# Kernel tuning notes

Hardware: AMD Instinct MI355X
Metric: run time of the kernel (lower is better)

## Reference

```python
import jax, jax.numpy as jnp
import numpy as np

WIN = 9  # window_size (isotropic, module default)
EPS = 1e-5


def _box_sum3d(x, win):
    """Sum over a win^3 box, same-size output ('same' padding). x: [B,1,D,H,W].
    The ones kernel is separable, so apply three 1D convolutions."""
    pad = win // 2
    for ax in range(3):  # spatial axes D,H,W
        kshape = [1, 1, 1, 1, 1]
        kshape[2 + ax] = win
        k = jnp.ones(kshape, x.dtype)
        padding = [(0, 0)] * 3
        padding[ax] = (pad, pad)
        x = jax.lax.conv_general_dilated(x, k, window_strides=(1, 1, 1), padding=padding)
    return x


def setup_inputs() -> dict:
    key = jax.random.key(0)
    k1, k2 = jax.random.split(key)
    shape = (2, 1, 160, 192, 160)
    y_pred = jax.random.normal(k1, shape, dtype=jnp.float32)
    y_true = jax.random.normal(k2, shape, dtype=jnp.float32)
    return {"y_pred": y_pred, "y_true": y_true}


def reference(y_pred, y_true):
    I, J = y_true, y_pred
    win_size = jnp.asarray(WIN ** 3, I.dtype)  # 729

    I_sum = _box_sum3d(I, WIN)
    J_sum = _box_sum3d(J, WIN)
    I2_sum = _box_sum3d(I * I, WIN)
    J2_sum = _box_sum3d(J * J, WIN)
    IJ_sum = _box_sum3d(I * J, WIN)

    I_mean = I_sum / win_size
    J_mean = J_sum / win_size

    cross = IJ_sum - J_mean * I_sum - I_mean * J_sum + I_mean * J_mean * win_size
    I_var = I2_sum - 2 * I_mean * I_sum + I_mean * I_mean * win_size
    J_var = J2_sum - 2 * J_mean * J_sum + J_mean * J_mean * win_size

    cc = cross * cross / (I_var * J_var + EPS)
    return -jnp.mean(cc)
```

## Files before the change

### kernel.cpp

```cpp
#include <hip/hip_runtime.h>


#define B_    2
#define D_    160
#define H_    192
#define W_    160
#define HW_   (H_*W_)
#define SSTR  28
#define SSLC  (24*SSTR)
#define OFF_J (2*SSLC)
#define OFF_WS 2688
#define WFS   484
#define WSLC5 (5*WFS)
#define OFF_HS (OFF_WS + 2*WSLC5)
#define HFS   324
#define HSLC5 (5*HFS)
#define OFF_RED (OFF_HS + 2*HSLC5)
#define SMEM_TOT (OFF_RED + 8)
#define DC    40
#define NMAC  24
#define W3I   (1.0f/729.0f)
#define NTOT  9830400.0f

#if __has_builtin(__builtin_amdgcn_rcpf)
#define RCP(x) __builtin_amdgcn_rcpf(x)
#else
#define RCP(x) (1.0f/(x))
#endif

#define LGKM0() asm volatile("s_waitcnt lgkmcnt(0)" ::: "memory")

#define SLIDEX(EXPR, F) { \
  float v_[12]; \
  _Pragma("unroll") for (int k_ = 0; k_ < 12; ++k_) { v_[k_] = (EXPR); } \
  float s_ = v_[0]+v_[1]+v_[2]+v_[3]+v_[4]+v_[5]+v_[6]+v_[7]+v_[8]; \
  float4 o_; o_.x = s_; s_ += v_[9]-v_[0]; o_.y = s_; \
  s_ += v_[10]-v_[1]; o_.z = s_; s_ += v_[11]-v_[2]; o_.w = s_; \
  *(float4*)&sm[wwr + (F)*WFS] = o_; }

__global__ __launch_bounds__(256, 3) void ncc_fused(const float* __restrict__ gI,
                                                    const float* __restrict__ gJ,
                                                    float* __restrict__ out)
{
  __shared__ __align__(16) float sm[SMEM_TOT];
  const int tid  = threadIdx.x;
  const int lane = tid & 63;
  const int Q    = tid >> 6;
  const int w0   = blockIdx.x * 16;
  const int h0   = blockIdx.y * 16;
  const int bz   = blockIdx.z;
  const int bb   = bz >> 2;
  const int d_lo = (bz & 3) * DC;

  for (int i = tid; i < OFF_WS; i += 256) sm[i] = 0.f;

  bool val0 = false, val1 = false;
  int  lds0 = 0, lds1 = 0, slc0 = 0, slc1 = 0;
  const float *pi0 = gI, *pj0 = gJ, *pi1 = gI, *pj1 = gJ;
  {
    const int tA = tid;
    const int tB = (tid >= 224) ? (tid + 32) : 512;
    auto prep = [&](int t, bool& val, int& lo, int& slc,
                    const float*& pi, const float*& pj) {
      if (t >= 288) { val = false; return; }
      slc = t / 144;
      const int u = t - slc*144;
      const int r = u / 6, c = u - r*6;
      const int gh = h0 - 4 + r;
      const int gw = w0 - 4 + 4*c;
      val = ((unsigned)gh < (unsigned)H_) && (gw >= 0) && (gw + 3 < W_);
      lo  = slc*SSLC + r*SSTR + 4*c;
      const long off = ((long)(bb*D_ + (d_lo - 4 + slc))*H_ + gh)*(long)W_ + gw;
      pi = gI + off; pj = gJ + off;
    };
    prep(tA, val0, lds0, slc0, pi0, pj0);
    prep(tB, val1, lds1, slc1, pi1, pj1);
  }

  const bool wact = (lane < 48);
  const int  wslc = lane / 24;
  const int  wrow = lane - wslc*24;
  const int  wrd  = wslc*SSLC + wrow*SSTR + 4*Q;
  const int  wwr  = OFF_WS + wslc*WSLC5 + wrow*20 + 4*Q;

  auto prep_h = [&](int t, int& rd, int& wr) {
    const int wq   = t & 3;
    const int f    = (t >> 2) % 5;
    const int half = (t / 20) & 1;
    const int slc  = t / 40;
    rd = OFF_WS + slc*WSLC5 + f*WFS + half*160 + 4*Q + wq;
    wr = OFF_HS + slc*HSLC5 + f*HFS + half*160 + 4*Q + wq;
  };
  int h1rd, h1wr, h2rd = 0, h2wr = 0;
  prep_h(lane, h1rd, h1wr);
  const bool hact2 = (lane < 16);
  if (hact2) prep_h(lane + 64, h2rd, h2wr);

  const int rh = lane >> 2, rwq = lane & 3;
  const int hbA = OFF_HS + rh*20 + 4*Q + rwq;
  const int hbB = hbA + HSLC5;

  float ring[5][9], S[5];
  #pragma unroll
  for (int f = 0; f < 5; ++f) {
    S[f] = 0.f;
    #pragma unroll
    for (int k = 0; k < 9; ++k) ring[f][k] = 0.f;
  }
  float acc = 0.f;

  float4 f0i = {0,0,0,0}, f0j = {0,0,0,0}, f1i = {0,0,0,0}, f1j = {0,0,0,0};
  auto fetch = [&](int sbase) {
    if (val0 && (unsigned)(sbase + slc0) < (unsigned)D_) {
      f0i = *(const float4*)pi0; f0j = *(const float4*)pj0;
    } else { f0i = make_float4(0,0,0,0); f0j = make_float4(0,0,0,0); }
    pi0 += 2*HW_; pj0 += 2*HW_;
    if (val1 && (unsigned)(sbase + slc1) < (unsigned)D_) {
      f1i = *(const float4*)pi1; f1j = *(const float4*)pj1;
    } else { f1i = make_float4(0,0,0,0); f1j = make_float4(0,0,0,0); }
    pi1 += 2*HW_; pj1 += 2*HW_;
  };
  auto stage_write = [&]() {
    if (val0) { *(float4*)&sm[lds0] = f0i; *(float4*)&sm[lds0 + OFF_J] = f0j; }
    if (val1) { *(float4*)&sm[lds1] = f1i; *(float4*)&sm[lds1 + OFF_J] = f1j; }
  };

  auto ring_cc = [&](int mu) {
    float nA[5], nB[5];
    #pragma unroll
    for (int f = 0; f < 5; ++f) { nA[f] = sm[hbA + f*HFS]; nB[f] = sm[hbB + f*HFS]; }
    float SA[5], SB[5];
    #pragma unroll
    for (int f = 0; f < 5; ++f) {
      SA[f] = S[f]  + nA[f] - ring[f][8];
      SB[f] = SA[f] + nB[f] - ring[f][7];
      S[f]  = SB[f];
      #pragma unroll
      for (int k = 8; k >= 2; --k) ring[f][k] = ring[f][k-2];
      ring[f][1] = nA[f]; ring[f][0] = nB[f];
    }
    if (mu >= 4) {
      {
        const float cr = SA[4] - SA[0]*SA[1]*W3I;
        const float vi = SA[2] - SA[0]*SA[0]*W3I;
        const float vj = SA[3] - SA[1]*SA[1]*W3I;
        acc += cr*cr * RCP(vi*vj + 1e-5f);
      }
      {
        const float cr = SB[4] - SB[0]*SB[1]*W3I;
        const float vi = SB[2] - SB[0]*SB[0]*W3I;
        const float vj = SB[3] - SB[1]*SB[1]*W3I;
        acc += cr*cr * RCP(vi*vj + 1e-5f);
      }
    }
  };

  fetch(d_lo - 4);
  __syncthreads();
  stage_write();
  __syncthreads();

  int sA = d_lo - 4;
  for (int m = 0; m < NMAC; ++m, sA += 2) {
    if (m + 1 < NMAC) fetch(sA + 2);

    if (m > 0) ring_cc(m - 1);

    if (wact) {
      const float4 a0 = *(const float4*)&sm[wrd];
      const float4 a1 = *(const float4*)&sm[wrd + 4];
      const float4 a2 = *(const float4*)&sm[wrd + 8];
      const float4 b0 = *(const float4*)&sm[wrd + OFF_J];
      const float4 b1 = *(const float4*)&sm[wrd + OFF_J + 4];
      const float4 b2 = *(const float4*)&sm[wrd + OFF_J + 8];
      const float wi[12] = {a0.x,a0.y,a0.z,a0.w,a1.x,a1.y,a1.z,a1.w,a2.x,a2.y,a2.z,a2.w};
      const float wj[12] = {b0.x,b0.y,b0.z,b0.w,b1.x,b1.y,b1.z,b1.w,b2.x,b2.y,b2.z,b2.w};
      SLIDEX(wi[k_],        0)
      SLIDEX(wj[k_],        1)
      SLIDEX(wi[k_]*wi[k_], 2)
      SLIDEX(wj[k_]*wj[k_], 3)
      SLIDEX(wi[k_]*wj[k_], 4)
    }
    LGKM0();

    {
      auto hrun = [&](int rd, int wr) {
        float v[16];
        #pragma unroll
        for (int k = 0; k < 16; ++k) v[k] = sm[rd + k*20];
        float s = v[0]+v[1]+v[2]+v[3]+v[4]+v[5]+v[6]+v[7]+v[8];
        sm[wr] = s;
        #pragma unroll
        for (int j = 1; j < 8; ++j) { s += v[j+8] - v[j-1]; sm[wr + j*20] = s; }
      };
      hrun(h1rd, h1wr);
      if (hact2) hrun(h2rd, h2wr);
    }

    __syncthreads();
    if (m + 1 < NMAC) stage_write();
    __syncthreads();
  }

  ring_cc(NMAC - 1);

  float v = acc;
  #pragma unroll
  for (int off = 32; off > 0; off >>= 1)
    v += __shfl_down(v, off, 64);
  if (lane == 0) sm[OFF_RED + Q] = v;
  __syncthreads();
  if (tid == 0) {
    const float t = sm[OFF_RED] + sm[OFF_RED+1] + sm[OFF_RED+2] + sm[OFF_RED+3];
    atomicAdd(out, -t / NTOT);
  }
}

extern "C" void kernel_launch(void* const* d_in, const int* in_sizes, int n_in,
                              void* d_out, int out_size, void* d_ws, size_t ws_size,
                              hipStream_t stream) {
  const float* J = (const float*)d_in[0];
  const float* I = (const float*)d_in[1];
  float* outp = (float*)d_out;
  hipMemsetAsync(d_out, 0, sizeof(float), stream);
  dim3 grid(W_/16, H_/16, B_*4);
  ncc_fused<<<grid, dim3(256), 0, stream>>>(I, J, outp);
}
```

Before: 174.6 us.

## Store W/H partial box sums as fp16 in LDS and use packed half2 H-pass

Converts the W-direction partial sums to packed fp16 before writing them to shared memory. The H-direction sliding sum now runs with packed half2 add/sub on fewer lanes, and the D-ring reads back single halves. The D-ring/cc step moves into the same iteration right after the H pass, and launch bounds rise to 4 blocks/SM because LDS use shrinks. This cuts LDS footprint and traffic and halves H-pass ALU work. The cost is large precision loss: the I², J² and IJ sums and the variance subtractions lose accuracy in fp16, which may break the tolerance.

Result: faster. 151.3 us (-13.3%).

```diff
diff --git a/kernel.cpp b/kernel.cpp
--- a/kernel.cpp
+++ b/kernel.cpp
@@ -1,4 +1,5 @@
 #include <hip/hip_runtime.h>
+#include <hip/hip_fp16.h>
 
 
 #define B_    2
@@ -10,12 +11,14 @@
 #define SSLC  (24*SSTR)
 #define OFF_J (2*SSLC)
 #define OFF_WS 2688
-#define WFS   484
-#define WSLC5 (5*WFS)
-#define OFF_HS (OFF_WS + 2*WSLC5)
-#define HFS   324
-#define HSLC5 (5*HFS)
-#define OFF_RED (OFF_HS + 2*HSLC5)
+#define WROW  10
+#define WSLC2 240
+#define WFS2  486
+#define OFF_HS (OFF_WS + 5*WFS2)
+#define HROW  10
+#define HSLC2 160
+#define HFS2  326
+#define OFF_RED (OFF_HS + 5*HFS2)
 #define SMEM_TOT (OFF_RED + 8)
 #define DC    40
 #define NMAC  24
@@ -29,6 +32,8 @@
 #endif
 
 #define LGKM0() asm volatile("s_waitcnt lgkmcnt(0)" ::: "memory")
+
+struct __align__(8) Half2x2 { __half2 a, b; };
 
 #define SLIDEX(EXPR, F) { \
   float v_[12]; \
@@ -36,9 +41,11 @@
   float s_ = v_[0]+v_[1]+v_[2]+v_[3]+v_[4]+v_[5]+v_[6]+v_[7]+v_[8]; \
   float4 o_; o_.x = s_; s_ += v_[9]-v_[0]; o_.y = s_; \
   s_ += v_[10]-v_[1]; o_.z = s_; s_ += v_[11]-v_[2]; o_.w = s_; \
-  *(float4*)&sm[wwr + (F)*WFS] = o_; }
-
-__global__ __launch_bounds__(256, 3) void ncc_fused(const float* __restrict__ gI,
+  Half2x2 pk_; pk_.a = __floats2half2_rn(o_.x, o_.y); \
+  pk_.b = __floats2half2_rn(o_.z, o_.w); \
+  *(Half2x2*)&sm[wwr + (F)*WFS2] = pk_; }
+
+__global__ __launch_bounds__(256, 4) void ncc_fused(const float* __restrict__ gI,
                                                     const float* __restrict__ gJ,
                                                     float* __restrict__ out)
 {
@@ -78,27 +85,26 @@
   }
 
   const bool wact = (lane < 48);
-  const int  wslc = lane / 24;
-  const int  wrow = lane - wslc*24;
+  const int  wslc = (lane >= 24) ? 1 : 0;
+  const int  wrow = lane - 24*wslc;
   const int  wrd  = wslc*SSLC + wrow*SSTR + 4*Q;
-  const int  wwr  = OFF_WS + wslc*WSLC5 + wrow*20 + 4*Q;
-
-  auto prep_h = [&](int t, int& rd, int& wr) {
-    const int wq   = t & 3;
-    const int f    = (t >> 2) % 5;
-    const int half = (t / 20) & 1;
-    const int slc  = t / 40;
-    rd = OFF_WS + slc*WSLC5 + f*WFS + half*160 + 4*Q + wq;
-    wr = OFF_HS + slc*HSLC5 + f*HFS + half*160 + 4*Q + wq;
-  };
-  int h1rd, h1wr, h2rd = 0, h2wr = 0;
-  prep_h(lane, h1rd, h1wr);
-  const bool hact2 = (lane < 16);
-  if (hact2) prep_h(lane + 64, h2rd, h2wr);
+  const int  wwr  = OFF_WS + wslc*WSLC2 + wrow*WROW + 2*Q;
+
+  const bool hact = (lane < 40);
+  int hrd = 0, hwr = 0;
+  {
+    const int t     = hact ? lane : 0;
+    const int wpair = t & 1;
+    const int f     = (t >> 1) % 5;
+    const int half  = (t / 10) & 1;
+    const int slc   = t / 20;
+    hrd = OFF_WS + f*WFS2 + slc*WSLC2 + half*(8*WROW) + 2*Q + wpair;
+    hwr = OFF_HS + f*HFS2 + slc*HSLC2 + half*(8*HROW) + 2*Q + wpair;
+  }
 
   const int rh = lane >> 2, rwq = lane & 3;
-  const int hbA = OFF_HS + rh*20 + 4*Q + rwq;
-  const int hbB = hbA + HSLC5;
+  const int hb  = OFF_HS + rh*HROW + 2*Q + (rwq >> 1);
+  const int sh16 = (rwq & 1) * 16;
 
   float ring[5][9], S[5];
   #pragma unroll
@@ -125,34 +131,9 @@
     if (val1) { *(float4*)&sm[lds1] = f1i; *(float4*)&sm[lds1 + OFF_J] = f1j; }
   };
 
-  auto ring_cc = [&](int mu) {
-    float nA[5], nB[5];
-    #pragma unroll
-    for (int f = 0; f < 5; ++f) { nA[f] = sm[hbA + f*HFS]; nB[f] = sm[hbB + f*HFS]; }
-    float SA[5], SB[5];
-    #pragma unroll
-    for (int f = 0; f < 5; ++f) {
-      SA[f] = S[f]  + nA[f] - ring[f][8];
-      SB[f] = SA[f] + nB[f] - ring[f][7];
-      S[f]  = SB[f];
-      #pragma unroll
-      for (int k = 8; k >= 2; --k) ring[f][k] = ring[f][k-2];
-      ring[f][1] = nA[f]; ring[f][0] = nB[f];
-    }
-    if (mu >= 4) {
-      {
-        const float cr = SA[4] - SA[0]*SA[1]*W3I;
-        const float vi = SA[2] - SA[0]*SA[0]*W3I;
-        const float vj = SA[3] - SA[1]*SA[1]*W3I;
-        acc += cr*cr * RCP(vi*vj + 1e-5f);
-      }
-      {
-        const float cr = SB[4] - SB[0]*SB[1]*W3I;
-        const float vi = SB[2] - SB[0]*SB[0]*W3I;
-        const float vj = SB[3] - SB[1]*SB[1]*W3I;
-        acc += cr*cr * RCP(vi*vj + 1e-5f);
-      }
-    }
+  auto h2ext = [&](int addr) -> float {
+    const unsigned u = *(const unsigned*)&sm[addr];
+    return __half2float(__ushort_as_half((unsigned short)(u >> sh16)));
   };
 
   fetch(d_lo - 4);
@@ -163,8 +144,6 @@
   int sA = d_lo - 4;
   for (int m = 0; m < NMAC; ++m, sA += 2) {
     if (m + 1 < NMAC) fetch(sA + 2);
-
-    if (m > 0) ring_cc(m - 1);
 
     if (wact) {
       const float4 a0 = *(const float4*)&sm[wrd];
@@ -183,26 +162,60 @@
     }
     LGKM0();
 
+    if (hact) {
+      __half2 v[16];
+      #pragma unroll
+      for (int k = 0; k < 16; ++k) v[k] = *(const __half2*)&sm[hrd + k*WROW];
+      __half2 s = __hadd2(v[0], v[1]);
+      s = __hadd2(s, v[2]); s = __hadd2(s, v[3]); s = __hadd2(s, v[4]);
+      s = __hadd2(s, v[5]); s = __hadd2(s, v[6]); s = __hadd2(s, v[7]);
+      s = __hadd2(s, v[8]);
+      *(__half2*)&sm[hwr] = s;
+      #pragma unroll
+      for (int j = 1; j < 8; ++j) {
+        s = __hsub2(__hadd2(s, v[j+8]), v[j-1]);
+        *(__half2*)&sm[hwr + j*HROW] = s;
+      }
+    }
+    LGKM0();
+
     {
-      auto hrun = [&](int rd, int wr) {
-        float v[16];
+      float nA[5], nB[5];
+      #pragma unroll
+      for (int f = 0; f < 5; ++f) {
+        nA[f] = h2ext(hb + f*HFS2);
+        nB[f] = h2ext(hb + f*HFS2 + HSLC2);
+      }
+      float SA[5], SB[5];
+      #pragma unroll
+      for (int f = 0; f < 5; ++f) {
+        SA[f] = S[f]  + nA[f] - ring[f][8];
+        SB[f] = SA[f] + nB[f] - ring[f][7];
+        S[f]  = SB[f];
         #pragma unroll
-        for (int k = 0; k < 16; ++k) v[k] = sm[rd + k*20];
-        float s = v[0]+v[1]+v[2]+v[3]+v[4]+v[5]+v[6]+v[7]+v[8];
-        sm[wr] = s;
-        #pragma unroll
-        for (int j = 1; j < 8; ++j) { s += v[j+8] - v[j-1]; sm[wr + j*20] = s; }
-      };
-      hrun(h1rd, h1wr);
-      if (hact2) hrun(h2rd, h2wr);
+        for (int k = 8; k >= 2; --k) ring[f][k] = ring[f][k-2];
+        ring[f][1] = nA[f]; ring[f][0] = nB[f];
+      }
+      if (m >= 4) {
+        {
+          const float cr = SA[4] - SA[0]*SA[1]*W3I;
+          const float vi = SA[2] - SA[0]*SA[0]*W3I;
+          const float vj = SA[3] - SA[1]*SA[1]*W3I;
+          acc += cr*cr * RCP(vi*vj + 1e-5f);
+        }
+        {
+          const float cr = SB[4] - SB[0]*SB[1]*W3I;
+          const float vi = SB[2] - SB[0]*SB[0]*W3I;
+          const float vj = SB[3] - SB[1]*SB[1]*W3I;
+          acc += cr*cr * RCP(vi*vj + 1e-5f);
+        }
+      }
     }
 
     __syncthreads();
     if (m + 1 < NMAC) stage_write();
     __syncthreads();
   }
-
-  ring_cc(NMAC - 1);
 
   float v = acc;
   #pragma unroll
```

## Compute in-plane box sums with fp16 MFMA banded-matrix products

Applied to the files above, without the earlier changes.

Replaces the scalar sliding-window W and H box sums with 16x16x32 fp16 MFMA multiplications against a banded 0/1 selection matrix. Inputs and their products are converted to half precision when staged into shared memory, and intermediate sums are also kept in fp16. The goal is to move the dominant in-plane summation work onto matrix cores, shrink shared memory so occupancy can rise to 4 blocks, and double-buffer the global fetch across the loop. The cost is substantial precision loss: fp16 storage of squared values and of sums up to about 81 before variance subtraction risks catastrophic cancellation in the variance terms.

After: 147.5 us. 1.18x faster.

```diff
diff --git a/kernel.cpp b/kernel.cpp
--- a/kernel.cpp
+++ b/kernel.cpp
@@ -1,4 +1,5 @@
 #include <hip/hip_runtime.h>
+#include <hip/hip_fp16.h>
 
 
 #define B_    2
@@ -6,17 +7,18 @@
 #define H_    192
 #define W_    160
 #define HW_   (H_*W_)
-#define SSTR  28
-#define SSLC  (24*SSTR)
-#define OFF_J (2*SSLC)
-#define OFF_WS 2688
-#define WFS   484
-#define WSLC5 (5*WFS)
-#define OFF_HS (OFF_WS + 2*WSLC5)
-#define HFS   324
-#define HSLC5 (5*HFS)
-#define OFF_RED (OFF_HS + 2*HSLC5)
-#define SMEM_TOT (OFF_RED + 8)
+
+#define RS    20
+#define SLS   (24*RS)
+#define FS    (2*SLS)
+#define ZROW  4800
+#define TMP0  4816
+#define TS    20
+#define HSUM0 (TMP0 + 4*320)
+#define HCS   160
+#define HRS   10
+#define REDU  (HSUM0 + 10*HCS)
+#define SMEM  (REDU + 8)
 #define DC    40
 #define NMAC  24
 #define W3I   (1.0f/729.0f)
@@ -27,78 +29,74 @@
 #else
 #define RCP(x) (1.0f/(x))
 #endif
-
 #define LGKM0() asm volatile("s_waitcnt lgkmcnt(0)" ::: "memory")
 
-#define SLIDEX(EXPR, F) { \
-  float v_[12]; \
-  _Pragma("unroll") for (int k_ = 0; k_ < 12; ++k_) { v_[k_] = (EXPR); } \
-  float s_ = v_[0]+v_[1]+v_[2]+v_[3]+v_[4]+v_[5]+v_[6]+v_[7]+v_[8]; \
-  float4 o_; o_.x = s_; s_ += v_[9]-v_[0]; o_.y = s_; \
-  s_ += v_[10]-v_[1]; o_.z = s_; s_ += v_[11]-v_[2]; o_.w = s_; \
-  *(float4*)&sm[wwr + (F)*WFS] = o_; }
-
-__global__ __launch_bounds__(256, 3) void ncc_fused(const float* __restrict__ gI,
+typedef _Float16 half8 __attribute__((ext_vector_type(8)));
+typedef float    f32x4 __attribute__((ext_vector_type(4)));
+#define MFMA16(a,b,c) __builtin_amdgcn_mfma_f32_16x16x32_f16((a),(b),(c),0,0,0)
+
+struct __align__(8) HP { __half2 a, b; };
+
+__global__ __launch_bounds__(256, 4) void ncc_fused(const float* __restrict__ gI,
                                                     const float* __restrict__ gJ,
                                                     float* __restrict__ out)
 {
-  __shared__ __align__(16) float sm[SMEM_TOT];
+  __shared__ __align__(16) float sm[SMEM];
   const int tid  = threadIdx.x;
   const int lane = tid & 63;
   const int Q    = tid >> 6;
+  const int n15  = lane & 15;
+  const int q4   = lane >> 4;
   const int w0   = blockIdx.x * 16;
   const int h0   = blockIdx.y * 16;
   const int bz   = blockIdx.z;
   const int bb   = bz >> 2;
   const int d_lo = (bz & 3) * DC;
 
-  for (int i = tid; i < OFF_WS; i += 256) sm[i] = 0.f;
+  for (int i = tid; i < TMP0; i += 256) sm[i] = 0.f;
+
+  half8 SEL;
+  #pragma unroll
+  for (int j = 0; j < 8; ++j) {
+    const int k = 8*q4 + j;
+    SEL[j] = (k >= n15 && k <= n15 + 8) ? (_Float16)1 : (_Float16)0;
+  }
 
   bool val0 = false, val1 = false;
-  int  lds0 = 0, lds1 = 0, slc0 = 0, slc1 = 0;
+  int  lo0 = 0, lo1 = 0, sc0 = 0, sc1 = 0;
   const float *pi0 = gI, *pj0 = gJ, *pi1 = gI, *pj1 = gJ;
   {
-    const int tA = tid;
-    const int tB = (tid >= 224) ? (tid + 32) : 512;
-    auto prep = [&](int t, bool& val, int& lo, int& slc,
+    auto prep = [&](int t, bool& val, int& lo, int& sc,
                     const float*& pi, const float*& pj) {
       if (t >= 288) { val = false; return; }
-      slc = t / 144;
-      const int u = t - slc*144;
+      sc = t / 144;
+      const int u = t - sc*144;
       const int r = u / 6, c = u - r*6;
-      const int gh = h0 - 4 + r;
-      const int gw = w0 - 4 + 4*c;
+      const int gh = h0 - 4 + r, gw = w0 - 4 + 4*c;
       val = ((unsigned)gh < (unsigned)H_) && (gw >= 0) && (gw + 3 < W_);
-      lo  = slc*SSLC + r*SSTR + 4*c;
-      const long off = ((long)(bb*D_ + (d_lo - 4 + slc))*H_ + gh)*(long)W_ + gw;
+      lo  = sc*SLS + r*RS + 2*c;
+      const long off = ((long)(bb*D_ + (d_lo - 4 + sc))*H_ + gh)*(long)W_ + gw;
       pi = gI + off; pj = gJ + off;
     };
-    prep(tA, val0, lds0, slc0, pi0, pj0);
-    prep(tB, val1, lds1, slc1, pi1, pj1);
-  }
-
-  const bool wact = (lane < 48);
-  const int  wslc = lane / 24;
-  const int  wrow = lane - wslc*24;
-  const int  wrd  = wslc*SSLC + wrow*SSTR + 4*Q;
-  const int  wwr  = OFF_WS + wslc*WSLC5 + wrow*20 + 4*Q;
-
-  auto prep_h = [&](int t, int& rd, int& wr) {
-    const int wq   = t & 3;
-    const int f    = (t >> 2) % 5;
-    const int half = (t / 20) & 1;
-    const int slc  = t / 40;
-    rd = OFF_WS + slc*WSLC5 + f*WFS + half*160 + 4*Q + wq;
-    wr = OFF_HS + slc*HSLC5 + f*HFS + half*160 + 4*Q + wq;
-  };
-  int h1rd, h1wr, h2rd = 0, h2wr = 0;
-  prep_h(lane, h1rd, h1wr);
-  const bool hact2 = (lane < 16);
-  if (hact2) prep_h(lane + 64, h2rd, h2wr);
-
-  const int rh = lane >> 2, rwq = lane & 3;
-  const int hbA = OFF_HS + rh*20 + 4*Q + rwq;
-  const int hbB = hbA + HSLC5;
+    prep(tid, val0, lo0, sc0, pi0, pj0);
+    prep((tid >= 224) ? tid + 32 : 512, val1, lo1, sc1, pi1, pj1);
+  }
+
+  int rb_[3], hb_[3];
+  #pragma unroll
+  for (int i = 0; i < 3; ++i) {
+    int c = Q + 4*i; if (c > 9) c = 9;
+    rb_[i] = (c % 5)*FS + (c / 5)*SLS;
+    hb_[i] = HSUM0 + c*HCS;
+  }
+  const int tb  = TMP0 + Q*320 + n15*TS;
+  const int a1r = n15*RS + 4*q4;
+  const int a2r = (n15 < 8) ? ((16 + n15)*RS + 4*q4) : -1;
+  const int zr  = ZROW + 4*q4;
+
+  const int rh = tid >> 4, rw = tid & 15;
+  const int rbase = HSUM0 + rw*HRS + (rh >> 1);
+  const int rsh   = (rh & 1) * 16;
 
   float ring[5][9], S[5];
   #pragma unroll
@@ -111,24 +109,66 @@
 
   float4 f0i = {0,0,0,0}, f0j = {0,0,0,0}, f1i = {0,0,0,0}, f1j = {0,0,0,0};
   auto fetch = [&](int sbase) {
-    if (val0 && (unsigned)(sbase + slc0) < (unsigned)D_) {
+    if (val0 && (unsigned)(sbase + sc0) < (unsigned)D_) {
       f0i = *(const float4*)pi0; f0j = *(const float4*)pj0;
     } else { f0i = make_float4(0,0,0,0); f0j = make_float4(0,0,0,0); }
     pi0 += 2*HW_; pj0 += 2*HW_;
-    if (val1 && (unsigned)(sbase + slc1) < (unsigned)D_) {
+    if (val1 && (unsigned)(sbase + sc1) < (unsigned)D_) {
       f1i = *(const float4*)pi1; f1j = *(const float4*)pj1;
     } else { f1i = make_float4(0,0,0,0); f1j = make_float4(0,0,0,0); }
     pi1 += 2*HW_; pj1 += 2*HW_;
   };
+
+  auto stage_one = [&](int lo, float4 fi, float4 fj) {
+    const __half2 i01 = __floats2half2_rn(fi.x, fi.y);
+    const __half2 i23 = __floats2half2_rn(fi.z, fi.w);
+    const __half2 j01 = __floats2half2_rn(fj.x, fj.y);
+    const __half2 j23 = __floats2half2_rn(fj.z, fj.w);
+    HP hI; hI.a = i01; hI.b = i23;
+    HP hJ; hJ.a = j01; hJ.b = j23;
+    HP h2; h2.a = __hmul2(i01, i01); h2.b = __hmul2(i23, i23);
+    HP h3; h3.a = __hmul2(j01, j01); h3.b = __hmul2(j23, j23);
+    HP h4; h4.a = __hmul2(i01, j01); h4.b = __hmul2(i23, j23);
+    *(HP*)&sm[lo]        = hI;
+    *(HP*)&sm[lo +   FS] = hJ;
+    *(HP*)&sm[lo + 2*FS] = h2;
+    *(HP*)&sm[lo + 3*FS] = h3;
+    *(HP*)&sm[lo + 4*FS] = h4;
+  };
   auto stage_write = [&]() {
-    if (val0) { *(float4*)&sm[lds0] = f0i; *(float4*)&sm[lds0 + OFF_J] = f0j; }
-    if (val1) { *(float4*)&sm[lds1] = f1i; *(float4*)&sm[lds1 + OFF_J] = f1j; }
-  };
-
-  auto ring_cc = [&](int mu) {
+    if (val0) stage_one(lo0, f0i, f0j);
+    if (val1) stage_one(lo1, f1i, f1j);
+  };
+
+  auto chain = [&](int rb, int hb) {
+    const half8 A1 = *(const half8*)&sm[rb + a1r];
+    const half8 A2 = (a2r >= 0) ? *(const half8*)&sm[rb + a2r]
+                                : *(const half8*)&sm[zr];
+    const f32x4 z = {0.f, 0.f, 0.f, 0.f};
+    const f32x4 d1 = MFMA16(A1, SEL, z);
+    const f32x4 d2 = MFMA16(A2, SEL, z);
+    HP p1; p1.a = __floats2half2_rn(d1[0], d1[1]); p1.b = __floats2half2_rn(d1[2], d1[3]);
+    HP p2; p2.a = __floats2half2_rn(d2[0], d2[1]); p2.b = __floats2half2_rn(d2[2], d2[3]);
+    *(HP*)&sm[tb + 2*q4]     = p1;
+    *(HP*)&sm[tb + 8 + 2*q4] = p2;
+    LGKM0();
+    const half8 Bh = *(const half8*)&sm[tb + 4*q4];
+    const f32x4 dh = MFMA16(SEL, Bh, z);
+    HP ph; ph.a = __floats2half2_rn(dh[0], dh[1]); ph.b = __floats2half2_rn(dh[2], dh[3]);
+    *(HP*)&sm[hb + n15*HRS + 2*q4] = ph;
+  };
+
+  auto h2ext = [&](int addr) -> float {
+    const unsigned u = *(const unsigned*)&sm[addr];
+    return __half2float(__ushort_as_half((unsigned short)(u >> rsh)));
+  };
+  auto ring_cc = [&](int m) {
     float nA[5], nB[5];
     #pragma unroll
-    for (int f = 0; f < 5; ++f) { nA[f] = sm[hbA + f*HFS]; nB[f] = sm[hbB + f*HFS]; }
+    for (int f = 0; f < 5; ++f) {
+      nA[f] = h2ext(rbase + f*HCS);
+      nB[f] = h2ext(rbase + (5 + f)*HCS);
+    }
     float SA[5], SB[5];
     #pragma unroll
     for (int f = 0; f < 5; ++f) {
@@ -139,7 +179,7 @@
       for (int k = 8; k >= 2; --k) ring[f][k] = ring[f][k-2];
       ring[f][1] = nA[f]; ring[f][0] = nB[f];
     }
-    if (mu >= 4) {
+    if (m >= 4) {
       {
         const float cr = SA[4] - SA[0]*SA[1]*W3I;
         const float vi = SA[2] - SA[0]*SA[0]*W3I;
@@ -158,60 +198,27 @@
   fetch(d_lo - 4);
   __syncthreads();
   stage_write();
+  fetch(d_lo - 2);
   __syncthreads();
 
-  int sA = d_lo - 4;
-  for (int m = 0; m < NMAC; ++m, sA += 2) {
-    if (m + 1 < NMAC) fetch(sA + 2);
-
-    if (m > 0) ring_cc(m - 1);
-
-    if (wact) {
-      const float4 a0 = *(const float4*)&sm[wrd];
-      const float4 a1 = *(const float4*)&sm[wrd + 4];
-      const float4 a2 = *(const float4*)&sm[wrd + 8];
-      const float4 b0 = *(const float4*)&sm[wrd + OFF_J];
-      const float4 b1 = *(const float4*)&sm[wrd + OFF_J + 4];
-      const float4 b2 = *(const float4*)&sm[wrd + OFF_J + 8];
-      const float wi[12] = {a0.x,a0.y,a0.z,a0.w,a1.x,a1.y,a1.z,a1.w,a2.x,a2.y,a2.z,a2.w};
-      const float wj[12] = {b0.x,b0.y,b0.z,b0.w,b1.x,b1.y,b1.z,b1.w,b2.x,b2.y,b2.z,b2.w};
-      SLIDEX(wi[k_],        0)
-      SLIDEX(wj[k_],        1)
-      SLIDEX(wi[k_]*wi[k_], 2)
-      SLIDEX(wj[k_]*wj[k_], 3)
-      SLIDEX(wi[k_]*wj[k_], 4)
-    }
-    LGKM0();
-
-    {
-      auto hrun = [&](int rd, int wr) {
-        float v[16];
-        #pragma unroll
-        for (int k = 0; k < 16; ++k) v[k] = sm[rd + k*20];
-        float s = v[0]+v[1]+v[2]+v[3]+v[4]+v[5]+v[6]+v[7]+v[8];
-        sm[wr] = s;
-        #pragma unroll
-        for (int j = 1; j < 8; ++j) { s += v[j+8] - v[j-1]; sm[wr + j*20] = s; }
-      };
-      hrun(h1rd, h1wr);
-      if (hact2) hrun(h2rd, h2wr);
-    }
-
+  for (int m = 0; m < NMAC; ++m) {
+    chain(rb_[0], hb_[0]);
+    chain(rb_[1], hb_[1]);
+    if (Q < 2) chain(rb_[2], hb_[2]);
     __syncthreads();
-    if (m + 1 < NMAC) stage_write();
+    ring_cc(m);
+    if (m + 1 < NMAC) { stage_write(); fetch(d_lo + 2*m); }
     __syncthreads();
   }
-
-  ring_cc(NMAC - 1);
 
   float v = acc;
   #pragma unroll
   for (int off = 32; off > 0; off >>= 1)
     v += __shfl_down(v, off, 64);
-  if (lane == 0) sm[OFF_RED + Q] = v;
+  if (lane == 0) sm[REDU + Q] = v;
   __syncthreads();
   if (tid == 0) {
-    const float t = sm[OFF_RED] + sm[OFF_RED+1] + sm[OFF_RED+2] + sm[OFF_RED+3];
+    const float t = sm[REDU] + sm[REDU+1] + sm[REDU+2] + sm[REDU+3];
     atomicAdd(out, -t / NTOT);
   }
 }
```
